# Performance work log

Measured on AMD Instinct MI355X. Metric: run time of the kernel, lower is better.

## Reference

```python
import jax, jax.numpy as jnp
import numpy as np

B, T, N, F = 8, 24, 207, 16
H = 64            # hidden_dim
DH = 16           # dims_hyper[-1] / node-embedding out
DA = 4 * F        # temporal attention dim_out
DS = 64           # ss_gal gcn out dim (last_ss_gal_dim)
GDEP = 2
ALPHA, BETA, GAMMA = 0.05, 0.95, 0.95
TA = 2.0


def _lin(x, w, b=None):
    y = x @ w
    return y if b is None else y + b


def gcn_hyper(x, A, W, b):
    # x: [B,N,C], A: [N,N] static. h <- a*x + g * einsum('nvc,vw->nwc', h, A)
    h = x
    outs = [h]
    for _ in range(GDEP):
        h = ALPHA * x + GAMMA * jnp.einsum('bvc,vw->bwc', h, A)
        outs.append(h)
    return _lin(jnp.concatenate(outs, axis=-1), W, b)


def gcn_gru(x, A_dyn, A_sta, W, b):
    # x: [B,N,C], A_dyn: [B,N,N], A_sta: [N,N]
    h = x
    outs = [h]
    for _ in range(GDEP):
        h = (ALPHA * x
             + BETA * jnp.einsum('bvw,bvc->bwc', A_dyn, h)     # bmm(A^T, h)
             + GAMMA * jnp.einsum('bvc,vw->bwc', h, A_sta))
        outs.append(h)
    return _lin(jnp.concatenate(outs, axis=-1), W, b)


def gcn_ssgal(x, A, W, b):
    # x: [B*,N,C], A: [B*,N,N]
    h = x
    outs = [h]
    for _ in range(GDEP):
        h = ALPHA * x + GAMMA * jnp.einsum('bvw,bvc->bwc', A, h)
        outs.append(h)
    return _lin(jnp.concatenate(outs, axis=-1), W, b)


def setup_inputs() -> dict:
    key = jax.random.key(0)
    ks = jax.random.split(key, 32)
    i = iter(range(32))
    w = lambda *s: (0.02 * jax.random.normal(ks[next(i)], s, dtype=jnp.float32))
    inp = {
        'input_sequence': jax.random.normal(ks[next(i)], (B, T, N, F), dtype=jnp.float32),
        'static_adj': jax.random.uniform(ks[next(i)], (N, N), dtype=jnp.float32),
        # hyper graph generators: mlp in = (GDEP+1)*H -> DH
        'src_gen_w': w((GDEP + 1) * H, DH), 'src_gen_b': w(DH),
        'tgt_gen_w': w((GDEP + 1) * H, DH), 'tgt_gen_b': w(DH),
        # node embeddings: F -> DH
        'src_emb_w': w(F, DH), 'src_emb_b': w(DH),
        'tgt_emb_w': w(F, DH), 'tgt_emb_b': w(DH),
        # GRU gate GCNs: mlp in = (GDEP+1)*(F+H) -> H
        'gru_z_w': w((GDEP + 1) * (F + H), H), 'gru_z_b': w(H),
        'gru_r_w': w((GDEP + 1) * (F + H), H), 'gru_r_b': w(H),
        'gru_c_w': w((GDEP + 1) * (F + H), H), 'gru_c_b': w(H),
        # temporal attention: F -> DA, score DA -> 1
        'attn_q_w': w(F, DA),
        'attn_k_w': w(F, DA), 'attn_k_b': w(DA),
        'attn_s_w': w(DA, 1),
        # ss_gal spatial gcn: (GDEP+1)*F -> DS
        'sgcn_w': w((GDEP + 1) * F, DS), 'sgcn_b': w(DS),
        # predictors
        'short_w': w(DS, F), 'short_b': w(F),
        'long_w': w(H, F), 'long_b': w(F),
        'fus_w': w(DS + H, F), 'fus_b': w(F),
    }
    return inp


def _forward(input_sequence, static_adj,
             src_gen_w, src_gen_b, tgt_gen_w, tgt_gen_b,
             src_emb_w, src_emb_b, tgt_emb_w, tgt_emb_b,
             gru_z_w, gru_z_b, gru_r_w, gru_r_b, gru_c_w, gru_c_b,
             attn_q_w, attn_k_w, attn_k_b, attn_s_w,
             sgcn_w, sgcn_b,
             short_w, short_b, long_w, long_b, fus_w, fus_b):
    batch, steps, nodes = input_sequence.shape[0], input_sequence.shape[1], input_sequence.shape[2]
    eye = jnp.eye(nodes, dtype=input_sequence.dtype)

    def cell(x_t, h):
        # x_t: [B,N,F], h: [B,N,H]
        src_ctx = gcn_hyper(h, static_adj, src_gen_w, src_gen_b)   # [B,N,DH]
        tgt_ctx = gcn_hyper(h, static_adj, tgt_gen_w, tgt_gen_b)
        s = jnp.tanh(TA * _lin(x_t, src_emb_w, src_emb_b) * src_ctx)
        t = jnp.tanh(TA * _lin(x_t, tgt_emb_w, tgt_emb_b) * tgt_ctx)
        asym = jnp.einsum('bnc,bmc->bnm', s, t) - jnp.einsum('bnc,bmc->bnm', t, s)
        adj = jax.nn.relu(jnp.tanh(TA * asym)) + eye
        adj = adj / (adj.sum(axis=-1, keepdims=True) + 1e-8)
        gi = jnp.concatenate([x_t, h], axis=-1)
        z = jax.nn.sigmoid(gcn_gru(gi, adj, static_adj, gru_z_w, gru_z_b))
        r = jax.nn.sigmoid(gcn_gru(gi, adj, static_adj, gru_r_w, gru_r_b))
        ri = jnp.concatenate([x_t, r * h], axis=-1)
        c = jnp.tanh(gcn_gru(ri, adj, static_adj, gru_c_w, gru_c_b))
        return z * h + (1.0 - z) * c

    h = jnp.zeros((batch, nodes, H), dtype=input_sequence.dtype)
    for t_step in range(0, max(1, steps - 4), 4):
        h = cell(input_sequence[:, t_step], h)

    # ss_gal branch on the last 4 steps
    recent = input_sequence[:, -4:]            # [B,4,N,F]
    target = input_sequence[:, -1]             # [B,N,F]
    # temporal attention
    q = target @ attn_q_w                      # [B,N,DA]
    k = recent @ attn_k_w + attn_k_b           # [B,4,N,DA]
    scores = jnp.tanh(q[:, None, :, None, :] + k[:, :, None, :, :])  # [B,4,N,N,DA]
    scores = jnp.squeeze(scores @ attn_s_w, axis=-1)                  # [B,4,N,N]
    attn = jax.nn.softmax(scores, axis=-1)
    dyn_adj = static_adj[None] + attn.reshape(-1, nodes, nodes)       # [B*4,N,N]
    rh = recent.reshape(-1, nodes, recent.shape[-1])                  # [B*4,N,F]
    rh = gcn_ssgal(rh, dyn_adj, sgcn_w, sgcn_b)                       # [B*4,N,DS]
    rh = jax.nn.relu(rh.reshape(batch, -1, nodes, rh.shape[-1]))      # [B,4,N,DS]
    target = jnp.sum(rh, axis=1)                                       # [B,N,DS]

    short = _lin(target, short_w, short_b)      # [B,N,F]
    h = cell(short, h)                          # final GRU step on short-term prediction
    long = _lin(h, long_w, long_b)              # [B,N,F]
    fused = _lin(jnp.concatenate([target, h], axis=-1), fus_w, fus_b)  # [B,N,F]
    return jnp.stack([short, long, fused], axis=0)  # [3,B,N,F]


def reference(input_sequence, static_adj,
              src_gen_w, src_gen_b, tgt_gen_w, tgt_gen_b,
              src_emb_w, src_emb_b, tgt_emb_w, tgt_emb_b,
              gru_z_w, gru_z_b, gru_r_w, gru_r_b, gru_c_w, gru_c_b,
              attn_q_w, attn_k_w, attn_k_b, attn_s_w,
              sgcn_w, sgcn_b,
              short_w, short_b, long_w, long_b, fus_w, fus_b):
    return _forward(input_sequence, static_adj,
                    src_gen_w, src_gen_b, tgt_gen_w, tgt_gen_b,
                    src_emb_w, src_emb_b, tgt_emb_w, tgt_emb_b,
                    gru_z_w, gru_z_b, gru_r_w, gru_r_b, gru_c_w, gru_c_b,
                    attn_q_w, attn_k_w, attn_k_b, attn_s_w,
                    sgcn_w, sgcn_b,
                    short_w, short_b, long_w, long_b, fus_w, fus_b)
```

## Files before the change

### kernel.cpp

```cpp
#include <hip/hip_runtime.h>


constexpr int B = 8, T = 24, N = 207, F = 16, H = 64, DH = 16;
constexpr int PS = 208;
constexpr float ALPHA = 0.05f, BETA = 0.95f, GAMMA = 0.95f, TA = 2.0f;
constexpr int NF = N * F;
constexpr int BNF = B * N * F;

__device__ __forceinline__ float tanh_fast(float x) { float e = __expf(2.f * x); return 1.f - 2.f / (e + 1.f); }
__device__ __forceinline__ float sigm(float x) { return 1.f / (1.f + __expf(-x)); }
__device__ __forceinline__ float tanh_poly(float x) {
    float x2 = x * x;
    float c = __builtin_fmaf(x2, 0.13333333f, -0.33333333f);
    return x * __builtin_fmaf(x2, c, 1.f);
}

__global__ __launch_bounds__(256) void k_stage0(
    const float* __restrict__ adj, const float* __restrict__ inp,
    const float* __restrict__ Wq, const float* __restrict__ Wk,
    const float* __restrict__ kb, const float* __restrict__ sw_,
    const float* __restrict__ Wes, const float* __restrict__ bes,
    const float* __restrict__ Wet, const float* __restrict__ bet,
    const float* __restrict__ bsrc, const float* __restrict__ btgt,
    float* __restrict__ Ts, float* __restrict__ A2,
    float* __restrict__ attnT, float* __restrict__ rsum,
    float* __restrict__ s_out, float* __restrict__ t_out, float* __restrict__ catg)
{
    __shared__ __align__(16) float smem[7424];
    int bid = blockIdx.x, tid = threadIdx.x;
    if (bid < 49) {
        int vb = (bid % 7) * 32, wb = (bid / 7) * 32;
        float* sA = smem;
        float* sB = smem + 1056;
        float acc[4] = {0, 0, 0, 0};
        int i0 = tid >> 5, j = tid & 31;
        for (int u0 = 0; u0 < N; u0 += 32) {
            __syncthreads();
            for (int l = tid; l < 1024; l += 256) {
                int i = l >> 5, jj = l & 31;
                int v = vb + i, u = u0 + jj;
                sA[i * 33 + jj] = (v < N && u < N) ? adj[v * N + u] : 0.f;
                int uu = u0 + i, w = wb + jj;
                sB[i * 33 + jj] = (uu < N && w < N) ? adj[uu * N + w] : 0.f;
            }
            __syncthreads();
#pragma unroll 8
            for (int u = 0; u < 32; u++) {
                float bv = sB[u * 33 + j];
#pragma unroll
                for (int k = 0; k < 4; k++) acc[k] += sA[(i0 + k * 8) * 33 + u] * bv;
            }
        }
#pragma unroll
        for (int k = 0; k < 4; k++) {
            int v = vb + i0 + k * 8, w = wb + j;
            if (v < N && w < N) A2[(size_t)w * PS + v] = acc[k];
        }
    } else if (bid < 217) {
        int i = (bid - 49) * 256 + tid;
        if (i < N * N) {
            int w = i / N, v = i % N;
            Ts[(size_t)w * PS + v] = adj[v * N + w];
        }
    } else if (bid < 1785) {
        int idx = bid - 217;
        int bt = idx / 49, rem = idx % 49;
        int n0 = (rem % 7) * 32, m0 = (rem / 7) * 32;
        int b = bt >> 2, tau = bt & 3;
        int ti = tid >> 4, tj = tid & 15;
        float* sQ = smem;
        float* sK = smem + 2080;
        float* sWq = smem + 4160;
        float* sWk = smem + 5184;
        float* sXq = smem + 6208;
        float* sXk = smem + 6752;
        float* ssw = smem + 7296;
        float* skb = smem + 7360;
        const float* xq = inp + ((size_t)(b * T + (T - 1))) * NF;
        const float* xk = inp + ((size_t)(b * T + 20 + tau)) * NF;
        {
            float4 wq4 = *(const float4*)&Wq[tid * 4];
            float4 wk4 = *(const float4*)&Wk[tid * 4];
            *(float4*)&sWq[(tid >> 4) * 64 + (tid & 15) * 4] = wq4;
            *(float4*)&sWk[(tid >> 4) * 64 + (tid & 15) * 4] = wk4;
            if (tid < 64) { ssw[tid] = sw_[tid]; skb[tid] = kb[tid]; }
            int i2 = tid & 127;
            int r = i2 >> 2, c4 = (i2 & 3) * 4;
            if (tid < 128) {
                float4 aq = make_float4(0, 0, 0, 0);
                int n = n0 + r;
                if (n < N) aq = *(const float4*)&xq[(size_t)n * F + c4];
                sXq[r * 17 + c4] = aq.x; sXq[r * 17 + c4 + 1] = aq.y; sXq[r * 17 + c4 + 2] = aq.z; sXq[r * 17 + c4 + 3] = aq.w;
            } else {
                float4 ck = make_float4(0, 0, 0, 0);
                int m = m0 + r;
                if (m < N) ck = *(const float4*)&xk[(size_t)m * F + c4];
                sXk[r * 17 + c4] = ck.x; sXk[r * 17 + c4 + 1] = ck.y; sXk[r * 17 + c4 + 2] = ck.z; sXk[r * 17 + c4 + 3] = ck.w;
            }
        }
        __syncthreads();
        {
            int r = tid >> 3, o0 = (tid & 7) * 8;
            float xr[16], xkr[16];
#pragma unroll
            for (int f = 0; f < 16; f++) { xr[f] = sXq[r * 17 + f]; xkr[f] = sXk[r * 17 + f]; }
#pragma unroll
            for (int j = 0; j < 8; j++) {
                int o = o0 + j;
                float aq = 0.f, ak = skb[o];
#pragma unroll
                for (int f = 0; f < 16; f++) { aq += xr[f] * sWq[f * 64 + o]; ak += xkr[f] * sWk[f * 64 + o]; }
                sQ[r * 65 + o] = aq; sK[r * 65 + o] = ak;
            }
        }
        __syncthreads();
        float s00 = 0.f, s01 = 0.f, s10 = 0.f, s11 = 0.f;
#pragma unroll 2
        for (int d = 0; d < 64; d++) {
            float w = ssw[d];
            float q1 = sQ[ti * 65 + d], q2 = sQ[(ti + 16) * 65 + d];
            float k1 = sK[tj * 65 + d], k2 = sK[(tj + 16) * 65 + d];
            s00 += tanh_poly(q1 + k1) * w;
            s01 += tanh_poly(q1 + k2) * w;
            s10 += tanh_poly(q2 + k1) * w;
            s11 += tanh_poly(q2 + k2) * w;
        }
        int n1 = n0 + ti, n2 = n0 + ti + 16, m1 = m0 + tj, m2 = m0 + tj + 16;
        bool vn1 = n1 < N, vn2 = n2 < N, vm1 = m1 < N, vm2 = m2 < N;
        float e00 = (vn1 && vm1) ? __expf(s00) : 0.f;
        float e01 = (vn1 && vm2) ? __expf(s01) : 0.f;
        float e10 = (vn2 && vm1) ? __expf(s10) : 0.f;
        float e11 = (vn2 && vm2) ? __expf(s11) : 0.f;
        float part1 = e00 + e01, part2 = e10 + e11;
        for (int d = 8; d > 0; d >>= 1) {
            part1 += __shfl_down(part1, d, 16);
            part2 += __shfl_down(part2, d, 16);
        }
        if (tj == 0) {
            if (vn1) atomicAdd(&rsum[bt * N + n1], part1);
            if (vn2) atomicAdd(&rsum[bt * N + n2], part2);
        }
        __syncthreads();
        float* tile = sQ;
        tile[tj * 33 + ti] = e00;
        tile[(tj + 16) * 33 + ti] = e01;
        tile[tj * 33 + ti + 16] = e10;
        tile[(tj + 16) * 33 + ti + 16] = e11;
        __syncthreads();
        {
            int row = tid >> 3, c4 = (tid & 7) * 4;
            int m = m0 + row;
            if (m < N) {
                float4 v = make_float4(tile[row * 33 + c4], tile[row * 33 + c4 + 1],
                                       tile[row * 33 + c4 + 2], tile[row * 33 + c4 + 3]);
                *(float4*)&attnT[(size_t)bt * PS * PS + (size_t)m * PS + n0 + c4] = v;
            }
        }
    } else {
        int idx = bid - 1785;
        int x13 = idx % 13, b = idx / 13;
        int w0 = x13 * 16;
        int ty = tid >> 4, tx = tid & 15;
        float* sX  = smem;
        float* sWs = smem + 272;
        float* sWt = smem + 528;
        const float* xp = inp + ((size_t)(b * T + 0)) * NF;
        {
            int w = w0 + ty;
            sX[ty * 17 + tx] = (w < N) ? xp[(size_t)w * F + tx] : 0.f;
            sWs[ty * 16 + tx] = Wes[ty * 16 + tx];
            sWt[ty * 16 + tx] = Wet[ty * 16 + tx];
        }
        __syncthreads();
        float xs = bes[tx], xt = bet[tx];
#pragma unroll
        for (int f = 0; f < 16; f++) {
            float xv = sX[ty * 17 + f];
            xs += xv * sWs[f * 16 + tx];
            xt += xv * sWt[f * 16 + tx];
        }
        int w = w0 + ty;
        if (w < N) {
            s_out[((size_t)(b * N + w)) * DH + tx] = tanh_fast(TA * xs * bsrc[tx]);
            t_out[((size_t)(b * N + w)) * DH + tx] = tanh_fast(TA * xt * btgt[tx]);
            catg[((size_t)(b * N + w)) * 80 + tx] = sX[ty * 17 + tx];
#pragma unroll
            for (int j = 0; j < 4; j++) catg[((size_t)(b * N + w)) * 80 + 16 + tx * 4 + j] = 0.f;
        }
    }
}

__global__ __launch_bounds__(256) void k_cell_a(
    const float* __restrict__ h, const float* __restrict__ Ts, const float* __restrict__ A2,
    const float* __restrict__ xseq, int tsel, const float* __restrict__ xbuf,
    const float* __restrict__ Wsrc, const float* __restrict__ bsrc,
    const float* __restrict__ Wtgt, const float* __restrict__ btgt,
    const float* __restrict__ Wes, const float* __restrict__ bes,
    const float* __restrict__ Wet, const float* __restrict__ bet,
    float* __restrict__ s_out, float* __restrict__ t_out, float* __restrict__ catg) {
    int b = blockIdx.y, w0 = blockIdx.x * 16, lane = blockIdx.z;
    int tid = threadIdx.x, ty = tid >> 4, tx = tid & 15;
    __shared__ float sTs[2][16][33], sA2[2][16][33];
    __shared__ float sH[2][32][64];
    __shared__ float cat[16][193];
    __shared__ float sW[192][16];
    __shared__ float sX[16][16], sWe[16][16];
    float au[4] = {0, 0, 0, 0}, aw[4] = {0, 0, 0, 0};
    const float* hb = h + b * N * H;
    const float* xp = (tsel >= 0) ? (xseq + ((size_t)(b * T + tsel)) * NF) : (xbuf + (size_t)b * NF);
    int pidx = tid & 127;
    int pr = pidx >> 3, pc4 = (pidx & 7) * 4;
    float4 t4;
    float4 h4[2];
    int hr[2], hc[2];
#pragma unroll
    for (int k = 0; k < 2; k++) { int l4 = tid + k * 256; hr[k] = l4 >> 4; hc[k] = (l4 & 15) * 4; }
    auto loadT = [&](int v0) {
        t4 = make_float4(0, 0, 0, 0);
        const float* src = (tid < 128) ? Ts : A2;
        int w = w0 + pr;
        if (w < N) t4 = *(const float4*)&src[(size_t)w * PS + v0 + pc4];
#pragma unroll
        for (int k = 0; k < 2; k++) {
            float4 hv = make_float4(0, 0, 0, 0);
            int v = v0 + hr[k];
            if (v < N) hv = *(const float4*)&hb[(size_t)v * H + hc[k]];
            h4[k] = hv;
        }
    };
    loadT(0);
    int cur = 0;
    for (int t = 0; t < 7; t++) {
        __syncthreads();
        {
            float (*dst)[33] = (tid < 128) ? sTs[cur] : sA2[cur];
            dst[pr][pc4] = t4.x; dst[pr][pc4 + 1] = t4.y; dst[pr][pc4 + 2] = t4.z; dst[pr][pc4 + 3] = t4.w;
        }
#pragma unroll
        for (int k = 0; k < 2; k++) *(float4*)&sH[cur][hr[k]][hc[k]] = h4[k];
        if (t < 6) loadT((t + 1) * 32);
        __syncthreads();
#pragma unroll 8
        for (int v = 0; v < 32; v++) {
            float pu = sTs[cur][ty][v], pw = sA2[cur][ty][v];
#pragma unroll
            for (int j = 0; j < 4; j++) {
                float x = sH[cur][v][tx * 4 + j];
                au[j] += pu * x; aw[j] += pw * x;
            }
        }
        cur ^= 1;
    }
    int w = w0 + ty;
    bool valid = w < N;
    __syncthreads();
    if (valid) {
#pragma unroll
        for (int j = 0; j < 4; j++) {
            int c = tx * 4 + j;
            float hv = hb[(size_t)w * H + c];
            float u = au[j], w2 = aw[j];
            cat[ty][c] = hv;
            cat[ty][64 + c] = ALPHA * hv + GAMMA * u;
            cat[ty][128 + c] = ALPHA * hv + ALPHA * GAMMA * u + GAMMA * GAMMA * w2;
        }
    } else {
#pragma unroll
        for (int j = 0; j < 4; j++) {
            int c = tx * 4 + j;
            cat[ty][c] = 0; cat[ty][64 + c] = 0; cat[ty][128 + c] = 0;
        }
    }
    const float* Wg = lane ? Wtgt : Wsrc;
    const float* bg = lane ? btgt : bsrc;
    const float* We = lane ? Wet : Wes;
    const float* be = lane ? bet : bes;
    {
        float4 wv[3];
#pragma unroll
        for (int k = 0; k < 3; k++) wv[k] = *(const float4*)&Wg[(tid + k * 256) * 4];
        float4 xv = make_float4(0, 0, 0, 0), ev = make_float4(0, 0, 0, 0);
        int sr = 0, sc = 0;
        if (tid < 64) {
            sr = tid >> 2; sc = (tid & 3) * 4;
            int n = w0 + sr;
            if (n < N) xv = *(const float4*)&xp[(size_t)n * F + sc];
            ev = *(const float4*)&We[tid * 4];
        }
#pragma unroll
        for (int k = 0; k < 3; k++) {
            int l4 = tid + k * 256;
            int r = l4 >> 2, c4 = (l4 & 3) * 4;
            *(float4*)&sW[r][c4] = wv[k];
        }
        if (tid < 64) {
            *(float4*)&sX[sr][sc] = xv;
            *(float4*)&sWe[sr][sc] = ev;
        }
    }
    __syncthreads();
    if (lane == 0 && valid) {
#pragma unroll
        for (int j = 0; j < 5; j++) {
            int c = tx * 5 + j;
            float v = (c < 16) ? sX[ty][c] : hb[(size_t)w * H + (c - 16)];
            catg[((size_t)(b * N + w)) * 80 + c] = v;
        }
    }
    {
        float ctx = bg[tx];
#pragma unroll 8
        for (int c = 0; c < 192; c++) ctx += cat[ty][c] * sW[c][tx];
        float xe = be[tx];
#pragma unroll
        for (int f = 0; f < 16; f++) xe += sX[ty][f] * sWe[f][tx];
        if (valid) {
            float val = tanh_fast(TA * xe * ctx);
            if (lane == 0) s_out[(size_t)(b * N + w) * DH + tx] = val;
            else           t_out[(size_t)(b * N + w) * DH + tx] = val;
        }
    }
}

__global__ __launch_bounds__(256) void k_cell_bP(const float* __restrict__ s_in, const float* __restrict__ t_in,
                                                 const float* __restrict__ adj, float* __restrict__ P) {
    int b = blockIdx.y, v0 = blockIdx.x * 8;
    int tid = threadIdx.x, ty = tid >> 5, tx = tid & 31;
    __shared__ float sS[N][17], sT[N][17];
    for (int l4 = tid; l4 < 828; l4 += 256) {
        float4 sv = *(const float4*)&s_in[(size_t)b * N * 16 + l4 * 4];
        float4 tv = *(const float4*)&t_in[(size_t)b * N * 16 + l4 * 4];
        int r = l4 >> 2, c = (l4 & 3) * 4;
        sS[r][c] = sv.x; sS[r][c + 1] = sv.y; sS[r][c + 2] = sv.z; sS[r][c + 3] = sv.w;
        sT[r][c] = tv.x; sT[r][c + 1] = tv.y; sT[r][c + 2] = tv.z; sT[r][c + 3] = tv.w;
    }
    __syncthreads();
    int v = v0 + ty;
    bool valid = v < N;
    int vc = valid ? v : (N - 1);
    float sv[16], tv[16];
#pragma unroll
    for (int k = 0; k < 16; k++) { sv[k] = sS[vc][k]; tv[k] = sT[vc][k]; }
    float val[7];
    float rsum = 0.f;
#pragma unroll
    for (int idx = 0; idx < 7; idx++) {
        int w = tx + 32 * idx;
        float r = 0.f;
        if (w < N) {
            float a = 0.f;
#pragma unroll
            for (int k = 0; k < 16; k++) a += sv[k] * sT[w][k] - tv[k] * sS[w][k];
            r = tanh_fast(TA * a);
            r = r > 0.f ? r : 0.f;
            if (w == v) r += 1.f;
        }
        val[idx] = r;
        rsum += r;
    }
    float tot = rsum;
    for (int d = 16; d > 0; d >>= 1) tot += __shfl_down(tot, d, 32);
    tot = __shfl(tot, 0, 32);
    float rinv = BETA / (tot + 1e-8f);
    if (valid) {
        float* Pb = P + (size_t)b * PS * PS;
#pragma unroll
        for (int idx = 0; idx < 7; idx++) {
            int w = tx + 32 * idx;
            if (w < N) Pb[(size_t)w * PS + v] = val[idx] * rinv + GAMMA * adj[v * N + w];
        }
    }
}

__device__ __forceinline__ void body_prop_xr(float* smem, int w0, int bt,
    const float* __restrict__ attnT, const float* __restrict__ rsum,
    const float* __restrict__ Ts, const float* __restrict__ inp, float* __restrict__ x1)
{
    int b = bt >> 2, tau = bt & 3;
    const float* xb = inp + ((size_t)(b * T + 20 + tau)) * NF;
    const float* PA = attnT + (size_t)bt * PS * PS;
    int tid = threadIdx.x, ty = tid >> 4, tx = tid & 15;
    float (*sPA)[16][33] = (float(*)[16][33])(smem);
    float (*sPT)[16][33] = (float(*)[16][33])(smem + 1056);
    float (*sX)[32][17]  = (float(*)[32][17])(smem + 2112);
    float (*sXs)[32][17] = (float(*)[32][17])(smem + 3200);
    float accA = 0.f, accT = 0.f;
    int prr = tid >> 3, pcc = (tid & 7) * 4;
    int xrr = (tid - 128) >> 2, xcc = ((tid - 128) & 3) * 4;
    float4 pa, pt, xv;
    float rinv_;
    auto loadT = [&](int v0) {
        pa = make_float4(0, 0, 0, 0); pt = make_float4(0, 0, 0, 0); xv = make_float4(0, 0, 0, 0); rinv_ = 0.f;
        if (tid < 128) {
            int w = w0 + prr;
            if (w < N) {
                pa = *(const float4*)&PA[(size_t)w * PS + v0 + pcc];
                pt = *(const float4*)&Ts[(size_t)w * PS + v0 + pcc];
            }
        } else {
            int v = v0 + xrr;
            if (v < N) {
                xv = *(const float4*)&xb[(size_t)v * F + xcc];
                rinv_ = __builtin_amdgcn_rcpf(rsum[bt * N + v]);
            }
        }
    };
    loadT(0);
    int cur = 0;
    for (int t = 0; t < 7; t++) {
        __syncthreads();
        if (tid < 128) {
            sPA[cur][prr][pcc] = pa.x; sPA[cur][prr][pcc + 1] = pa.y; sPA[cur][prr][pcc + 2] = pa.z; sPA[cur][prr][pcc + 3] = pa.w;
            sPT[cur][prr][pcc] = pt.x; sPT[cur][prr][pcc + 1] = pt.y; sPT[cur][prr][pcc + 2] = pt.z; sPT[cur][prr][pcc + 3] = pt.w;
        } else {
            sX[cur][xrr][xcc] = xv.x; sX[cur][xrr][xcc + 1] = xv.y; sX[cur][xrr][xcc + 2] = xv.z; sX[cur][xrr][xcc + 3] = xv.w;
            sXs[cur][xrr][xcc] = xv.x * rinv_; sXs[cur][xrr][xcc + 1] = xv.y * rinv_;
            sXs[cur][xrr][xcc + 2] = xv.z * rinv_; sXs[cur][xrr][xcc + 3] = xv.w * rinv_;
        }
        if (t < 6) loadT((t + 1) * 32);
        __syncthreads();
#pragma unroll 8
        for (int v = 0; v < 32; v++) {
            accA += sPA[cur][ty][v] * sXs[cur][v][tx];
            accT += sPT[cur][ty][v] * sX[cur][v][tx];
        }
        cur ^= 1;
    }
    int w = w0 + ty;
    if (w < N) x1[((size_t)(bt * N + w)) * 16 + tx] = ALPHA * xb[w * F + tx] + GAMMA * (accA + accT);
}

__device__ __forceinline__ void body_sgc2(float* smem, int w0, int bt,
    const float* __restrict__ attnT, const float* __restrict__ rsum,
    const float* __restrict__ Ts, const float* __restrict__ x1, const float* __restrict__ inp,
    const float* __restrict__ Ws, const float* __restrict__ bs, float* __restrict__ target)
{
    int b = bt >> 2, tau = bt & 3;
    const float* xb = inp + ((size_t)(b * T + 20 + tau)) * NF;
    const float* PA = attnT + (size_t)bt * PS * PS;
    int tid = threadIdx.x, ty = tid >> 4, tx = tid & 15;
    float (*sPA)[16][33] = (float(*)[16][33])(smem);
    float (*sPT)[16][33] = (float(*)[16][33])(smem + 1056);
    float (*sX)[32][17]  = (float(*)[32][17])(smem + 2112);
    float (*sXs)[32][17] = (float(*)[32][17])(smem + 3200);
    float (*scat)[48]    = (float(*)[48])(smem + 4288);
    float (*sWs)[64]     = (float(*)[64])(smem + 5056);
    float accA = 0.f, accT = 0.f;
    int prr = tid >> 3, pcc = (tid & 7) * 4;
    int xrr = (tid - 128) >> 2, xcc = ((tid - 128) & 3) * 4;
    float4 pa, pt, xv;
    float rinv_;
    auto loadT = [&](int v0) {
        pa = make_float4(0, 0, 0, 0); pt = make_float4(0, 0, 0, 0); xv = make_float4(0, 0, 0, 0); rinv_ = 0.f;
        if (tid < 128) {
            int w = w0 + prr;
            if (w < N) {
                pa = *(const float4*)&PA[(size_t)w * PS + v0 + pcc];
                pt = *(const float4*)&Ts[(size_t)w * PS + v0 + pcc];
            }
        } else {
            int v = v0 + xrr;
            if (v < N) {
                xv = *(const float4*)&x1[((size_t)(bt * N + v)) * 16 + xcc];
                rinv_ = __builtin_amdgcn_rcpf(rsum[bt * N + v]);
            }
        }
    };
    loadT(0);
    int cur = 0;
    for (int t = 0; t < 7; t++) {
        __syncthreads();
        if (tid < 128) {
            sPA[cur][prr][pcc] = pa.x; sPA[cur][prr][pcc + 1] = pa.y; sPA[cur][prr][pcc + 2] = pa.z; sPA[cur][prr][pcc + 3] = pa.w;
            sPT[cur][prr][pcc] = pt.x; sPT[cur][prr][pcc + 1] = pt.y; sPT[cur][prr][pcc + 2] = pt.z; sPT[cur][prr][pcc + 3] = pt.w;
        } else {
            sX[cur][xrr][xcc] = xv.x; sX[cur][xrr][xcc + 1] = xv.y; sX[cur][xrr][xcc + 2] = xv.z; sX[cur][xrr][xcc + 3] = xv.w;
            sXs[cur][xrr][xcc] = xv.x * rinv_; sXs[cur][xrr][xcc + 1] = xv.y * rinv_;
            sXs[cur][xrr][xcc + 2] = xv.z * rinv_; sXs[cur][xrr][xcc + 3] = xv.w * rinv_;
        }
        if (t < 6) loadT((t + 1) * 32);
        __syncthreads();
#pragma unroll 8
        for (int v = 0; v < 32; v++) {
            accA += sPA[cur][ty][v] * sXs[cur][v][tx];
            accT += sPT[cur][ty][v] * sX[cur][v][tx];
        }
        cur ^= 1;
    }
    int w = w0 + ty;
    bool valid = w < N;
    __syncthreads();
    for (int l = tid; l < 512; l += 256) {
        int i = l >> 5, c = l & 31;
        int ww = w0 + i;
        float vv = 0;
        if (ww < N) {
            if (c < 16) vv = xb[ww * F + c];
            else vv = x1[((size_t)bt * N + ww) * 16 + (c - 16)];
        }
        scat[i][c] = vv;
    }
    {
        float x0 = valid ? xb[w * F + tx] : 0.f;
        scat[ty][32 + tx] = ALPHA * x0 + GAMMA * (accA + accT);
    }
    {
        float4 wv[3];
#pragma unroll
        for (int k = 0; k < 3; k++) wv[k] = *(const float4*)&Ws[(tid + k * 256) * 4];
#pragma unroll
        for (int k = 0; k < 3; k++) {
            int l4 = tid + k * 256;
            *(float4*)&sWs[l4 >> 4][(l4 & 15) * 4] = wv[k];
        }
    }
    __syncthreads();
    float acc[4];
#pragma unroll
    for (int j = 0; j < 4; j++) acc[j] = bs[tx * 4 + j];
#pragma unroll 8
    for (int cc = 0; cc < 48; cc++) {
        float cv = scat[ty][cc];
        float4 w4 = *(const float4*)&sWs[cc][tx * 4];
        acc[0] += cv * w4.x; acc[1] += cv * w4.y; acc[2] += cv * w4.z; acc[3] += cv * w4.w;
    }
    if (valid) {
#pragma unroll
        for (int j = 0; j < 4; j++) {
            float r = acc[j] > 0.f ? acc[j] : 0.f;
            atomicAdd(&target[(b * N + w) * 64 + tx * 4 + j], r);
        }
    }
}

__device__ __forceinline__ void body_short(float* smem, int n0, int b,
    const float* __restrict__ target, const float* __restrict__ Wsh, const float* __restrict__ bsh,
    float* __restrict__ out, float* __restrict__ xshort)
{
    int tid = threadIdx.x, ty = tid >> 4, tx = tid & 15;
    float (*trow)[65] = (float(*)[65])(smem);
    float (*sW)[16]   = (float(*)[16])(smem + 1040);
    {
        int r = tid >> 4, c4 = (tid & 15) * 4;
        int n = n0 + r;
        float4 tv = make_float4(0, 0, 0, 0);
        if (n < N) tv = *(const float4*)&target[((size_t)(b * N + n)) * 64 + c4];
        trow[r][c4] = tv.x; trow[r][c4 + 1] = tv.y; trow[r][c4 + 2] = tv.z; trow[r][c4 + 3] = tv.w;
        float4 wv = *(const float4*)&Wsh[tid * 4];
        *(float4*)&sW[tid >> 2][(tid & 3) * 4] = wv;
    }
    __syncthreads();
    float acc = bsh[tx];
#pragma unroll 8
    for (int o = 0; o < 64; o++) acc += trow[ty][o] * sW[o][tx];
    int n = n0 + ty;
    if (n < N) {
        out[((size_t)0 * B * N + b * N + n) * 16 + tx] = acc;
        xshort[(b * N + n) * 16 + tx] = acc;
    }
}

__global__ __launch_bounds__(256) void k_psq(
    const float* __restrict__ P, float* __restrict__ P2, int aux,
    const float* __restrict__ attnT, const float* __restrict__ rsum,
    const float* __restrict__ Ts, const float* __restrict__ inp, float* __restrict__ x1,
    const float* __restrict__ Ws, const float* __restrict__ bs, float* __restrict__ target,
    const float* __restrict__ Wsh, const float* __restrict__ bsh,
    float* __restrict__ out, float* __restrict__ xshort)
{
    __shared__ __align__(16) float smem[8128];
    int bid = blockIdx.x, tid = threadIdx.x;
    if (bid < 1352) {
        int b = bid / 169, r = bid % 169;
        int w0 = (r % 13) * 16, v0 = (r / 13) * 16;
        const float* Pb = P + (size_t)b * PS * PS;
        float (*sA)[16][33] = (float(*)[16][33])(smem);
        float (*sB)[32][17] = (float(*)[32][17])(smem + 1056);
        int ty = tid >> 4, tx = tid & 15;
        int ar = tid >> 4, ac = (tid & 15) * 2;
        int br = tid >> 3, bc = (tid & 7) * 2;
        float2 av, bv;
        auto loadT = [&](int u0) {
            av = make_float2(0, 0); bv = make_float2(0, 0);
            int w = w0 + ar;
            if (w < N) av = *(const float2*)&Pb[(size_t)w * PS + u0 + ac];
            int u = u0 + br;
            if (u < N) bv = *(const float2*)&Pb[(size_t)u * PS + v0 + bc];
        };
        loadT(0);
        int cur = 0;
        float acc = 0.f;
        for (int t = 0; t < 7; t++) {
            __syncthreads();
            sA[cur][ar][ac] = av.x; sA[cur][ar][ac + 1] = av.y;
            sB[cur][br][bc] = bv.x; sB[cur][br][bc + 1] = bv.y;
            if (t < 6) loadT((t + 1) * 32);
            __syncthreads();
#pragma unroll 8
            for (int u = 0; u < 32; u++) acc += sA[cur][ty][u] * sB[cur][u][tx];
            cur ^= 1;
        }
        int w = w0 + ty, v = v0 + tx;
        if (w < N && v < N) P2[(size_t)b * PS * PS + (size_t)w * PS + v] = acc;
    } else {
        int idx = bid - 1352;
        if (aux == 1)      body_prop_xr(smem, (idx % 13) * 16, idx / 13, attnT, rsum, Ts, inp, x1);
        else if (aux == 2) body_sgc2(smem, (idx % 13) * 16, idx / 13, attnT, rsum, Ts, x1, inp, Ws, bs, target);
        else               body_short(smem, (idx % 13) * 16, idx / 13, target, Wsh, bsh, out, xshort);
    }
}

__global__ __launch_bounds__(256) void k_gate2(
    const float* __restrict__ cat, const float* __restrict__ P, const float* __restrict__ P2,
    const float* __restrict__ Wa, const float* __restrict__ ba,
    const float* __restrict__ Wb, const float* __restrict__ bb,
    int baseMode,
    const float* __restrict__ xseq, int tsel, const float* __restrict__ xbuf,
    float* __restrict__ zbuf, float* __restrict__ ricat,
    float* __restrict__ h,
    const float* __restrict__ target,
    const float* __restrict__ Wlong, const float* __restrict__ blong,
    const float* __restrict__ Wfus, const float* __restrict__ bfus,
    float* __restrict__ out) {
    int mode = baseMode + blockIdx.z;
    const float* W = (mode == 1) ? Wb : Wa;
    const float* bias = (mode == 1) ? bb : ba;
    int b = blockIdx.y, w0 = blockIdx.x * 16;
    int tid = threadIdx.x, ty = tid >> 4, tx = tid & 15;
    const float* Pb = P + (size_t)b * PS * PS;
    const float* Qb = P2 + (size_t)b * PS * PS;
    __shared__ float sC[16][241];
    __shared__ float sP[16][33], sQ[16][33];
    __shared__ float sX[32][81];
    __shared__ float sW[48][65];
    __shared__ float hrow[16][65], trow[16][65];
    for (int l4 = tid; l4 < 320; l4 += 256) {
        int r = l4 / 20, c4 = (l4 % 20) * 4;
        int w = w0 + r;
        float4 v4 = make_float4(0, 0, 0, 0);
        if (w < N) v4 = *(const float4*)&cat[((size_t)(b * N + w)) * 80 + c4];
        sC[r][c4] = v4.x; sC[r][c4 + 1] = v4.y; sC[r][c4 + 2] = v4.z; sC[r][c4 + 3] = v4.w;
    }
    float accP[5] = {0, 0, 0, 0, 0}, accQ[5] = {0, 0, 0, 0, 0};
    int prr = tid >> 4, prc = (tid & 15) * 2;
    int xrow = tid & 31, xc0 = (tid >> 5) * 10;
    float2 pv, qv;
    float2 xv[5];
    auto loadT = [&](int v0) {
        pv = make_float2(0, 0); qv = make_float2(0, 0);
        int w = w0 + prr;
        if (w < N) {
            pv = *(const float2*)&Pb[(size_t)w * PS + v0 + prc];
            qv = *(const float2*)&Qb[(size_t)w * PS + v0 + prc];
        }
        int v = v0 + xrow;
#pragma unroll
        for (int k = 0; k < 5; k++) xv[k] = make_float2(0, 0);
        if (v < N) {
            const float* src = &cat[((size_t)(b * N + v)) * 80 + xc0];
#pragma unroll
            for (int k = 0; k < 5; k++) xv[k] = *(const float2*)&src[k * 2];
        }
    };
    loadT(0);
    for (int t = 0; t < 7; t++) {
        __syncthreads();
        sP[prr][prc] = pv.x; sP[prr][prc + 1] = pv.y;
        sQ[prr][prc] = qv.x; sQ[prr][prc + 1] = qv.y;
#pragma unroll
        for (int k = 0; k < 5; k++) { sX[xrow][xc0 + 2 * k] = xv[k].x; sX[xrow][xc0 + 2 * k + 1] = xv[k].y; }
        if (t < 6) loadT((t + 1) * 32);
        __syncthreads();
#pragma unroll 8
        for (int v = 0; v < 32; v++) {
            float p = sP[ty][v], q = sQ[ty][v];
#pragma unroll
            for (int j = 0; j < 5; j++) {
                float x = sX[v][tx * 5 + j];
                accP[j] += p * x;
                accQ[j] += q * x;
            }
        }
    }
#pragma unroll
    for (int j = 0; j < 5; j++) {
        int c = tx * 5 + j;
        float g0 = sC[ty][c];
        sC[ty][80 + c]  = ALPHA * g0 + accP[j];
        sC[ty][160 + c] = ALPHA * g0 + ALPHA * accP[j] + accQ[j];
    }
    float4 wv[3];
#pragma unroll
    for (int k = 0; k < 3; k++) wv[k] = *(const float4*)&W[(tid + k * 256) * 4];
    float ga[4];
#pragma unroll
    for (int j = 0; j < 4; j++) ga[j] = bias[tx * 4 + j];
    for (int ch = 0; ch < 5; ch++) {
        __syncthreads();
#pragma unroll
        for (int k = 0; k < 3; k++) {
            int l4 = tid + k * 256;
            int r = l4 >> 4, cc = (l4 & 15) * 4;
            sW[r][cc] = wv[k].x; sW[r][cc + 1] = wv[k].y; sW[r][cc + 2] = wv[k].z; sW[r][cc + 3] = wv[k].w;
        }
        if (ch < 4) {
#pragma unroll
            for (int k = 0; k < 3; k++) wv[k] = *(const float4*)&W[(size_t)(ch + 1) * 3072 + (tid + k * 256) * 4];
        }
        __syncthreads();
        int c0 = ch * 48;
#pragma unroll 8
        for (int cc = 0; cc < 48; cc++) {
            float cv = sC[ty][c0 + cc];
#pragma unroll
            for (int j = 0; j < 4; j++) ga[j] += cv * sW[cc][tx * 4 + j];
        }
    }
    int w = w0 + ty;
    bool valid = w < N;
    if (mode == 0) {
        if (valid) {
#pragma unroll
            for (int j = 0; j < 4; j++) zbuf[((size_t)(b * N + w)) * 64 + tx * 4 + j] = sigm(ga[j]);
        }
    } else if (mode == 1) {
        if (valid) {
#pragma unroll
            for (int j = 0; j < 4; j++) {
                int o = tx * 4 + j;
                ricat[((size_t)(b * N + w)) * 80 + 16 + o] = sigm(ga[j]) * h[((size_t)(b * N + w)) * 64 + o];
            }
            if (tx < 4) {
                const float* xp = (tsel >= 0) ? (xseq + ((size_t)(b * T + tsel)) * NF) : (xbuf + (size_t)b * NF);
#pragma unroll
                for (int j = 0; j < 4; j++) {
                    int c = tx * 4 + j;
                    ricat[((size_t)(b * N + w)) * 80 + c] = xp[w * F + c];
                }
            }
        }
    } else {
#pragma unroll
        for (int j = 0; j < 4; j++) {
            int o = tx * 4 + j;
            float cval = tanh_fast(ga[j]);
            float zv = 0.f, hv = 0.f;
            if (valid) { zv = zbuf[((size_t)(b * N + w)) * 64 + o]; hv = h[((size_t)(b * N + w)) * 64 + o]; }
            float hn = zv * hv + (1.f - zv) * cval;
            if (valid) h[((size_t)(b * N + w)) * 64 + o] = hn;
            hrow[ty][o] = valid ? hn : 0.f;
        }
        if (mode == 3) {
            for (int l = tid; l < 1024; l += 256) {
                int i = l >> 6, o = l & 63;
                int ww = w0 + i;
                trow[i][o] = (ww < N) ? target[((size_t)(b * N + ww)) * 64 + o] : 0.f;
            }
            __syncthreads();
            float lg = blong[tx];
            float fs = bfus[tx];
#pragma unroll 8
            for (int o = 0; o < 64; o++) {
                lg += hrow[ty][o] * Wlong[o * 16 + tx];
                fs += trow[ty][o] * Wfus[o * 16 + tx] + hrow[ty][o] * Wfus[(64 + o) * 16 + tx];
            }
            if (valid) {
                out[((size_t)1 * B * N + b * N + w) * 16 + tx] = lg;
                out[((size_t)2 * B * N + b * N + w) * 16 + tx] = fs;
            }
        }
    }
}

extern "C" void kernel_launch(void* const* d_in, const int* in_sizes, int n_in,
                              void* d_out, int out_size, void* d_ws, size_t ws_size,
                              hipStream_t stream) {
    const float* inp = (const float*)d_in[0];
    const float* adj = (const float*)d_in[1];
    const float* src_gen_w = (const float*)d_in[2];
    const float* src_gen_b = (const float*)d_in[3];
    const float* tgt_gen_w = (const float*)d_in[4];
    const float* tgt_gen_b = (const float*)d_in[5];
    const float* src_emb_w = (const float*)d_in[6];
    const float* src_emb_b = (const float*)d_in[7];
    const float* tgt_emb_w = (const float*)d_in[8];
    const float* tgt_emb_b = (const float*)d_in[9];
    const float* gru_z_w = (const float*)d_in[10];
    const float* gru_z_b = (const float*)d_in[11];
    const float* gru_r_w = (const float*)d_in[12];
    const float* gru_r_b = (const float*)d_in[13];
    const float* gru_c_w = (const float*)d_in[14];
    const float* gru_c_b = (const float*)d_in[15];
    const float* attn_q_w = (const float*)d_in[16];
    const float* attn_k_w = (const float*)d_in[17];
    const float* attn_k_b = (const float*)d_in[18];
    const float* attn_s_w = (const float*)d_in[19];
    const float* sgcn_w = (const float*)d_in[20];
    const float* sgcn_b = (const float*)d_in[21];
    const float* short_w = (const float*)d_in[22];
    const float* short_b = (const float*)d_in[23];
    const float* long_w = (const float*)d_in[24];
    const float* long_b = (const float*)d_in[25];
    const float* fus_w = (const float*)d_in[26];
    const float* fus_b = (const float*)d_in[27];
    float* out = (float*)d_out;

    float* ws = (float*)d_ws;
    size_t off = 0;
    auto A = [&](size_t n) { n = (n + 3) & ~(size_t)3; float* p = ws + off; off += n; return p; };
    float* Ts = A((size_t)PS * PS);
    float* A2 = A((size_t)PS * PS);
    float* sbuf = A((size_t)B * N * DH);
    float* tbuf = A((size_t)B * N * DH);
    float* P = A((size_t)B * PS * PS);
    float* P2 = A((size_t)B * PS * PS);
    float* catg = A((size_t)B * N * 80);
    float* catc = A((size_t)B * N * 80);
    float* zb = A((size_t)B * N * 64);
    float* attnT = A((size_t)32 * PS * PS);
    float* x1 = A((size_t)32 * NF);
    float* xshort = A(BNF);
    size_t zero_begin = off;
    float* h = A((size_t)B * N * H);
    float* target = A((size_t)B * N * 64);
    float* rsum = A((size_t)32 * N);
    size_t zero_end = off;
    (void)ws_size; (void)in_sizes; (void)n_in; (void)out_size;

    hipMemsetAsync(h, 0, (zero_end - zero_begin) * sizeof(float), stream);
    k_stage0<<<1889, 256, 0, stream>>>(adj, inp, attn_q_w, attn_k_w, attn_k_b, attn_s_w,
                                       src_emb_w, src_emb_b, tgt_emb_w, tgt_emb_b,
                                       src_gen_b, tgt_gen_b,
                                       Ts, A2, attnT, rsum, sbuf, tbuf, catg);

    auto run_cell = [&](int tsel, const float* xbuf, int finalFlag, int aux, bool skipA) {
        if (!skipA)
            k_cell_a<<<dim3(13, B, 2), 256, 0, stream>>>(h, Ts, A2, inp, tsel, xbuf,
                                                         src_gen_w, src_gen_b, tgt_gen_w, tgt_gen_b,
                                                         src_emb_w, src_emb_b, tgt_emb_w, tgt_emb_b, sbuf, tbuf, catg);
        k_cell_bP<<<dim3(26, B), 256, 0, stream>>>(sbuf, tbuf, adj, P);
        int extra = (aux == 1 || aux == 2) ? 416 : (aux == 3 ? 104 : 0);
        k_psq<<<1352 + extra, 256, 0, stream>>>(P, P2, aux, attnT, rsum, Ts, inp, x1,
                                                sgcn_w, sgcn_b, target, short_w, short_b, out, xshort);
        k_gate2<<<dim3(13, B, 2), 256, 0, stream>>>(catg, P, P2, gru_z_w, gru_z_b, gru_r_w, gru_r_b, 0,
                                                    inp, tsel, xbuf, zb, catc, h,
                                                    nullptr, nullptr, nullptr, nullptr, nullptr, nullptr);
        k_gate2<<<dim3(13, B, 1), 256, 0, stream>>>(catc, P, P2, gru_c_w, gru_c_b, nullptr, nullptr, 2 + finalFlag,
                                                    nullptr, 0, nullptr, zb, nullptr, h,
                                                    target, long_w, long_b, fus_w, fus_b, out);
    };

    run_cell(0, nullptr, 0, 1, true);
    run_cell(4, nullptr, 0, 2, false);
    run_cell(8, nullptr, 0, 3, false);
    run_cell(12, nullptr, 0, 0, false);
    run_cell(16, nullptr, 0, 0, false);

    run_cell(-1, xshort, 1, 0, false);
}
```

Baseline: 606.5 us.

## Replace P-squared prerequisite for z/r gates with two-step P·(P·X) propagation

The z/r gate kernel no longer waits on P2 = P·P. A new kernel first computes P·cat for each batch, and the gate kernel then applies P to that result and builds the concatenated hop features before the weight GEMM. The P·P product now runs as extra blocks inside the gate launch, where its output is only needed by the later candidate kernel. This takes the dense square matmul off the critical path ahead of z/r and replaces it with cheaper skinny products. The cost is an extra intermediate buffer, and the hop-2 terms are now evaluated in a different order than before, which can change floating-point rounding.

```diff
diff --git a/kernel.cpp b/kernel.cpp
--- a/kernel.cpp
+++ b/kernel.cpp
@@ -560,8 +560,8 @@
     }
 }
 
-__global__ __launch_bounds__(256) void k_psq(
-    const float* __restrict__ P, float* __restrict__ P2, int aux,
+__global__ __launch_bounds__(256) void k_pg(
+    const float* __restrict__ P, const float* __restrict__ cat, float* __restrict__ pg, int aux,
     const float* __restrict__ attnT, const float* __restrict__ rsum,
     const float* __restrict__ Ts, const float* __restrict__ inp, float* __restrict__ x1,
     const float* __restrict__ Ws, const float* __restrict__ bs, float* __restrict__ target,
@@ -570,21 +570,184 @@
 {
     __shared__ __align__(16) float smem[8128];
     int bid = blockIdx.x, tid = threadIdx.x;
-    if (bid < 1352) {
-        int b = bid / 169, r = bid % 169;
+    if (bid < 520) {
+        int x13 = bid % 13, b = (bid / 13) & 7, z = bid / 104;
+        int w0 = x13 * 16, c0 = z * 16;
+        int ty = tid >> 4, tx = tid & 15;
+        const float* Pb = P + (size_t)b * PS * PS;
+        float (*sP)[16][33] = (float(*)[16][33])(smem);
+        float (*sX)[32][17] = (float(*)[32][17])(smem + 1056);
+        float a1 = 0.f;
+        int pr = tid >> 4, pc = (tid & 15) * 2;
+        int xr = tid >> 3, xc = (tid & 7) * 2;
+        float2 pv, xv;
+        auto loadT = [&](int v0) {
+            pv = make_float2(0, 0); xv = make_float2(0, 0);
+            int w = w0 + pr;
+            if (w < N) pv = *(const float2*)&Pb[(size_t)w * PS + v0 + pc];
+            int vv = v0 + xr;
+            if (vv < N) xv = *(const float2*)&cat[((size_t)(b * N + vv)) * 80 + c0 + xc];
+        };
+        loadT(0);
+        int cur = 0;
+        for (int t = 0; t < 7; t++) {
+            __syncthreads();
+            sP[cur][pr][pc] = pv.x; sP[cur][pr][pc + 1] = pv.y;
+            sX[cur][xr][xc] = xv.x; sX[cur][xr][xc + 1] = xv.y;
+            if (t < 6) loadT((t + 1) * 32);
+            __syncthreads();
+#pragma unroll 8
+            for (int v_ = 0; v_ < 32; v_++) a1 += sP[cur][ty][v_] * sX[cur][v_][tx];
+            cur ^= 1;
+        }
+        int w = w0 + ty;
+        if (w < N) pg[((size_t)(b * N + w)) * 80 + c0 + tx] = a1;
+    } else {
+        int idx = bid - 520;
+        if (aux == 1)      body_prop_xr(smem, (idx % 13) * 16, idx / 13, attnT, rsum, Ts, inp, x1);
+        else if (aux == 2) body_sgc2(smem, (idx % 13) * 16, idx / 13, attnT, rsum, Ts, x1, inp, Ws, bs, target);
+        else               body_short(smem, (idx % 13) * 16, idx / 13, target, Wsh, bsh, out, xshort);
+    }
+}
+
+__global__ __launch_bounds__(256) void k_gatezr(
+    const float* __restrict__ catg, const float* __restrict__ pg,
+    const float* __restrict__ P, float* __restrict__ P2,
+    const float* __restrict__ Wz, const float* __restrict__ bz,
+    const float* __restrict__ Wr, const float* __restrict__ br,
+    const float* __restrict__ xseq, int tsel, const float* __restrict__ xbuf,
+    float* __restrict__ zbuf, float* __restrict__ catc,
+    const float* __restrict__ h)
+{
+    __shared__ __align__(16) float smem[7504];
+    int bid = blockIdx.x, tid = threadIdx.x;
+    if (bid < 208) {
+        int mode = bid / 104, rem = bid % 104;
+        int x13 = rem % 13, b = rem / 13;
+        int w0 = x13 * 16;
+        int ty = tid >> 4, tx = tid & 15;
+        const float* W = mode ? Wr : Wz;
+        const float* bias = mode ? br : bz;
+        const float* Pb = P + (size_t)b * PS * PS;
+        float (*sC)[241] = (float(*)[241])(smem);
+        float (*sP)[33]  = (float(*)[33])(smem + 3856);
+        float (*sX)[81]  = (float(*)[81])(smem + 4384);
+        float (*sW)[65]  = (float(*)[65])(smem + 4384);
+        for (int l4 = tid; l4 < 320; l4 += 256) {
+            int r = l4 / 20, c4 = (l4 % 20) * 4;
+            int w = w0 + r;
+            float4 v4 = make_float4(0, 0, 0, 0);
+            if (w < N) v4 = *(const float4*)&catg[((size_t)(b * N + w)) * 80 + c4];
+            sC[r][c4] = v4.x; sC[r][c4 + 1] = v4.y; sC[r][c4 + 2] = v4.z; sC[r][c4 + 3] = v4.w;
+        }
+        float accP[5] = {0, 0, 0, 0, 0};
+        int prr = tid >> 4, prc = (tid & 15) * 2;
+        int xrow = tid & 31, xc0 = (tid >> 5) * 10;
+        float2 pv;
+        float2 xv[5];
+        auto loadT = [&](int v0) {
+            pv = make_float2(0, 0);
+            int w = w0 + prr;
+            if (w < N) pv = *(const float2*)&Pb[(size_t)w * PS + v0 + prc];
+            int v = v0 + xrow;
+#pragma unroll
+            for (int k = 0; k < 5; k++) xv[k] = make_float2(0, 0);
+            if (v < N) {
+                const float* src = &pg[((size_t)(b * N + v)) * 80 + xc0];
+#pragma unroll
+                for (int k = 0; k < 5; k++) xv[k] = *(const float2*)&src[k * 2];
+            }
+        };
+        loadT(0);
+        for (int t = 0; t < 7; t++) {
+            __syncthreads();
+            sP[prr][prc] = pv.x; sP[prr][prc + 1] = pv.y;
+#pragma unroll
+            for (int k = 0; k < 5; k++) { sX[xrow][xc0 + 2 * k] = xv[k].x; sX[xrow][xc0 + 2 * k + 1] = xv[k].y; }
+            if (t < 6) loadT((t + 1) * 32);
+            __syncthreads();
+#pragma unroll 8
+            for (int v = 0; v < 32; v++) {
+                float p = sP[ty][v];
+#pragma unroll
+                for (int j = 0; j < 5; j++) accP[j] += p * sX[v][tx * 5 + j];
+            }
+        }
+        int w = w0 + ty;
+        bool valid = w < N;
+#pragma unroll
+        for (int j = 0; j < 5; j++) {
+            int c = tx * 5 + j;
+            float pgo = valid ? pg[((size_t)(b * N + w)) * 80 + c] : 0.f;
+            float g0 = sC[ty][c];
+            sC[ty][80 + c]  = ALPHA * g0 + pgo;
+            sC[ty][160 + c] = ALPHA * g0 + ALPHA * pgo + accP[j];
+        }
+        float4 wv[3];
+#pragma unroll
+        for (int k = 0; k < 3; k++) wv[k] = *(const float4*)&W[(tid + k * 256) * 4];
+        float ga[4];
+#pragma unroll
+        for (int j = 0; j < 4; j++) ga[j] = bias[tx * 4 + j];
+        for (int ch = 0; ch < 5; ch++) {
+            __syncthreads();
+#pragma unroll
+            for (int k = 0; k < 3; k++) {
+                int l4 = tid + k * 256;
+                int r = l4 >> 4, cc = (l4 & 15) * 4;
+                sW[r][cc] = wv[k].x; sW[r][cc + 1] = wv[k].y; sW[r][cc + 2] = wv[k].z; sW[r][cc + 3] = wv[k].w;
+            }
+            if (ch < 4) {
+#pragma unroll
+                for (int k = 0; k < 3; k++) wv[k] = *(const float4*)&W[(size_t)(ch + 1) * 3072 + (tid + k * 256) * 4];
+            }
+            __syncthreads();
+            int c0 = ch * 48;
+#pragma unroll 8
+            for (int cc = 0; cc < 48; cc++) {
+                float cv = sC[ty][c0 + cc];
+#pragma unroll
+                for (int j = 0; j < 4; j++) ga[j] += cv * sW[cc][tx * 4 + j];
+            }
+        }
+        if (mode == 0) {
+            if (valid) {
+#pragma unroll
+                for (int j = 0; j < 4; j++) zbuf[((size_t)(b * N + w)) * 64 + tx * 4 + j] = sigm(ga[j]);
+            }
+        } else {
+            if (valid) {
+#pragma unroll
+                for (int j = 0; j < 4; j++) {
+                    int o = tx * 4 + j;
+                    catc[((size_t)(b * N + w)) * 80 + 16 + o] = sigm(ga[j]) * h[((size_t)(b * N + w)) * 64 + o];
+                }
+                if (tx < 4) {
+                    const float* xp = (tsel >= 0) ? (xseq + ((size_t)(b * T + tsel)) * NF) : (xbuf + (size_t)b * NF);
+#pragma unroll
+                    for (int j = 0; j < 4; j++) {
+                        int c = tx * 4 + j;
+                        catc[((size_t)(b * N + w)) * 80 + c] = xp[w * F + c];
+                    }
+                }
+            }
+        }
+    } else {
+        int idx = bid - 208;
+        int b = idx / 169, r = idx % 169;
         int w0 = (r % 13) * 16, v0 = (r / 13) * 16;
         const float* Pb = P + (size_t)b * PS * PS;
         float (*sA)[16][33] = (float(*)[16][33])(smem);
         float (*sB)[32][17] = (float(*)[32][17])(smem + 1056);
         int ty = tid >> 4, tx = tid & 15;
         int ar = tid >> 4, ac = (tid & 15) * 2;
-        int br = tid >> 3, bc = (tid & 7) * 2;
+        int br_ = tid >> 3, bc = (tid & 7) * 2;
         float2 av, bv;
         auto loadT = [&](int u0) {
             av = make_float2(0, 0); bv = make_float2(0, 0);
             int w = w0 + ar;
             if (w < N) av = *(const float2*)&Pb[(size_t)w * PS + u0 + ac];
-            int u = u0 + br;
+            int u = u0 + br_;
             if (u < N) bv = *(const float2*)&Pb[(size_t)u * PS + v0 + bc];
         };
         loadT(0);
@@ -593,7 +756,7 @@
         for (int t = 0; t < 7; t++) {
             __syncthreads();
             sA[cur][ar][ac] = av.x; sA[cur][ar][ac + 1] = av.y;
-            sB[cur][br][bc] = bv.x; sB[cur][br][bc + 1] = bv.y;
+            sB[cur][br_][bc] = bv.x; sB[cur][br_][bc + 1] = bv.y;
             if (t < 6) loadT((t + 1) * 32);
             __syncthreads();
 #pragma unroll 8
@@ -602,11 +765,6 @@
         }
         int w = w0 + ty, v = v0 + tx;
         if (w < N && v < N) P2[(size_t)b * PS * PS + (size_t)w * PS + v] = acc;
-    } else {
-        int idx = bid - 1352;
-        if (aux == 1)      body_prop_xr(smem, (idx % 13) * 16, idx / 13, attnT, rsum, Ts, inp, x1);
-        else if (aux == 2) body_sgc2(smem, (idx % 13) * 16, idx / 13, attnT, rsum, Ts, x1, inp, Ws, bs, target);
-        else               body_short(smem, (idx % 13) * 16, idx / 13, target, Wsh, bsh, out, xshort);
     }
 }
 
@@ -816,6 +974,7 @@
     float* P2 = A((size_t)B * PS * PS);
     float* catg = A((size_t)B * N * 80);
     float* catc = A((size_t)B * N * 80);
+    float* pgbuf = A((size_t)B * N * 80);
     float* zb = A((size_t)B * N * 64);
     float* attnT = A((size_t)32 * PS * PS);
     float* x1 = A((size_t)32 * NF);
@@ -840,11 +999,10 @@
                                                          src_emb_w, src_emb_b, tgt_emb_w, tgt_emb_b, sbuf, tbuf, catg);
         k_cell_bP<<<dim3(26, B), 256, 0, stream>>>(sbuf, tbuf, adj, P);
         int extra = (aux == 1 || aux == 2) ? 416 : (aux == 3 ? 104 : 0);
-        k_psq<<<1352 + extra, 256, 0, stream>>>(P, P2, aux, attnT, rsum, Ts, inp, x1,
-                                                sgcn_w, sgcn_b, target, short_w, short_b, out, xshort);
-        k_gate2<<<dim3(13, B, 2), 256, 0, stream>>>(catg, P, P2, gru_z_w, gru_z_b, gru_r_w, gru_r_b, 0,
-                                                    inp, tsel, xbuf, zb, catc, h,
-                                                    nullptr, nullptr, nullptr, nullptr, nullptr, nullptr);
+        k_pg<<<520 + extra, 256, 0, stream>>>(P, catg, pgbuf, aux, attnT, rsum, Ts, inp, x1,
+                                              sgcn_w, sgcn_b, target, short_w, short_b, out, xshort);
+        k_gatezr<<<1560, 256, 0, stream>>>(catg, pgbuf, P, P2, gru_z_w, gru_z_b, gru_r_w, gru_r_b,
+                                           inp, tsel, xbuf, zb, catc, h);
         k_gate2<<<dim3(13, B, 1), 256, 0, stream>>>(catc, P, P2, gru_c_w, gru_c_b, nullptr, nullptr, 2 + finalFlag,
                                                     nullptr, 0, nullptr, zb, nullptr, h,
                                                     target, long_w, long_b, fus_w, fus_b, out);
```

Result: faster. 589.7 us (median of 2 runs) (-2.8%).
